# Performance work log

Measured on AMD Instinct MI355X. Metric: run time of the kernel, lower is better.

The kernel has to match this reference:

```python
import jax, jax.numpy as jnp
import numpy as np

M = 65536
INPUT_DIM = 16
OUTPUT_DIM = 64
N = 32          # coordinates transformed by the spline
K = 16          # number of spline bins
MIN_BW = 0.001  # DEFAULT_MIN_BIN_WIDTH
MIN_BH = 0.001  # DEFAULT_MIN_BIN_HEIGHT


def setup_inputs() -> dict:
    key = jax.random.key(0)
    k1, k2, k3, k4 = jax.random.split(key, 4)
    c = jax.random.uniform(k1, (M, INPUT_DIM), jnp.float32)
    z = jax.random.uniform(k2, (M, OUTPUT_DIM), jnp.float32)  # data in [0,1] spline domain
    s_in = OUTPUT_DIM - N + INPUT_DIM  # 48
    s_out = N * (2 * K + 1)            # 1056
    W = jax.random.normal(k3, (s_in, s_out), jnp.float32) * 0.05
    b = jax.random.normal(k4, (s_out,), jnp.float32) * 0.05
    return {"c": c, "z": z, "W": W, "b": b}


def _quadratic_spline(inputs, unnormalized_widths, unnormalized_heights):
    # inputs: [m, n] in [0,1]; unnormalized_widths: [m, n, K]; unnormalized_heights: [m, n, K+1]
    num_bins = unnormalized_widths.shape[-1]

    widths = jax.nn.softmax(unnormalized_widths, axis=-1)
    widths = MIN_BW + (1.0 - MIN_BW * num_bins) * widths

    h = jax.nn.softplus(unnormalized_heights) + 0.001  # [m, n, K+1]
    # (heights have K+1 = num_bins+1 knots, so the 'num_bins-1' padding branch is skipped)
    area = jnp.sum((h[..., :-1] + h[..., 1:]) * 0.5 * widths, axis=-1, keepdims=True)
    heights = h / area
    heights = MIN_BH + (1.0 - MIN_BH) * heights

    cdf = jnp.cumsum((heights[..., :-1] + heights[..., 1:]) * 0.5 * widths, axis=-1)
    cdf = cdf.at[..., -1].set(1.0)
    bin_left_cdf = jnp.pad(cdf, ((0, 0), (0, 0), (1, 0)))  # [m, n, K+1]

    locs = jnp.cumsum(widths, axis=-1).at[..., -1].set(1.0)
    bin_locations = jnp.pad(locs, ((0, 0), (0, 0), (1, 0)))  # [m, n, K+1]

    # nflows torchutils.searchsorted: bump last knot by eps, count knots <= input
    locs_eps = bin_locations.at[..., -1].add(1e-6)
    bin_idx = jnp.sum(inputs[..., None] >= locs_eps, axis=-1) - 1  # [m, n] int

    def gather(arr, idx):
        return jnp.take_along_axis(arr, idx[..., None], axis=-1)[..., 0]

    input_bin_locations = gather(bin_locations, bin_idx)
    input_bin_widths = gather(widths, bin_idx)
    input_left_cdf = gather(bin_left_cdf, bin_idx)
    input_left_heights = gather(heights, bin_idx)
    input_right_heights = gather(heights, bin_idx + 1)

    a = 0.5 * (input_right_heights - input_left_heights) * input_bin_widths
    bq = input_left_heights * input_bin_widths
    cq = input_left_cdf

    alpha = (inputs - input_bin_locations) / input_bin_widths
    outputs = jnp.clip(a * alpha ** 2 + bq * alpha + cq, 0.0, 1.0)
    logabsdet = jnp.log(alpha * (input_right_heights - input_left_heights) + input_left_heights)
    return outputs, logabsdet


def reference(c, z, W, b):
    # forward (reverse=False) branch of QuadraticsSpline.forward
    z1, z2 = z[:, :N], z[:, N:]
    z2c = jnp.concatenate([z2, c], axis=1)
    y = z2c @ W + b                                  # conditioner s (linear)
    sv = y.reshape(y.shape[0], N, 2 * K + 1)
    unnormalized_heights = sv[..., : K + 1]          # first split chunk (size K+1)
    unnormalized_widths = sv[..., K + 1:]            # second chunk (size K)
    x1, log_det = _quadratic_spline(z1, unnormalized_widths, unnormalized_heights)
    x = jnp.concatenate([z2, x1], axis=1)            # note: original concatenates (x2, x1)
    return x, log_det.sum(axis=1)
```

## Files before the change

### kernel.cpp

```cpp
#include <hip/hip_runtime.h>
#include <hip/hip_bf16.h>
#include <math.h>

#define M_ROWS 65536
#define NSPLINE 32
#define BM 64
#define WROWS 16
#define GROUP 4
#define SPB 16
#define NITER (SPB / GROUP)
#define SLOT 40
#define WSLOT (64 * SLOT)
#define WB_ELEMS (32 * 3 * 2 * 64 * 8)

typedef __attribute__((ext_vector_type(8))) _Float16 half8;
typedef __attribute__((ext_vector_type(4))) _Float16 half4;
typedef __attribute__((ext_vector_type(4))) float floatx4;

__device__ __forceinline__ float softplus_fast(float t) {
    float u = t * t;
    float p = fmaf(u, 2.135645e-6f, -2.63517e-5f);
    p = fmaf(u, p, 3.4722222e-4f);
    p = fmaf(u, p, -5.2083333e-3f);
    p = fmaf(u, p, 0.125f);
    p = fmaf(u, p, 0.69314718f);
    return fmaf(t, 0.5f, p);
}

__global__ void pack_W(const float* __restrict__ W, const float* __restrict__ b,
                       _Float16* __restrict__ WH, float* __restrict__ out) {
    int idx = blockIdx.x * 256 + threadIdx.x;
    if (idx < M_ROWS) out[(size_t)M_ROWS * 64 + idx] = 0.0f;
    int j    = idx & 7;
    int lane = (idx >> 3) & 63;
    int half = (idx >> 9) & 1;
    int tmp  = idx >> 10;
    int t    = tmp % 3;
    int sp   = tmp / 3;
    int k  = half * 32 + ((lane >> 4) << 3) + j;
    int cl = t * 16 + (lane & 15);
    float v = 0.0f;
    if (cl < 33 && k <= 48) {
        int col = sp * 33 + cl;
        v = (k < 48) ? W[k * 1056 + col] : b[col];
    }
    WH[idx] = (_Float16)v;
}

__global__ void __launch_bounds__(256) fused_kernel(
    const float* __restrict__ z, const float* __restrict__ c,
    const _Float16* __restrict__ WH, float* __restrict__ out)
{
    __shared__ _Float16 lds[4 * WSLOT];

    const int tid  = threadIdx.x;
    const int w    = tid >> 6;
    const int lane = tid & 63;
    const int q    = lane >> 4;
    const int cc   = lane & 15;
    const int row_base = blockIdx.x * BM + w * WROWS;
    const int sp_base  = blockIdx.y * SPB;
    _Float16* mainA = lds + w * WSLOT;

    if (blockIdx.y == 0) {
        #pragma unroll
        for (int it = 0; it < 2; ++it) {
            int idx = it * 64 + lane;
            int rr  = row_base + (idx >> 3);
            int v4  = idx & 7;
            float4 val = *(const float4*)(z + (size_t)rr * 64 + 32 + v4 * 4);
            *(float4*)(out + (size_t)rr * 64 + v4 * 4) = val;
        }
    }

    half8 a0, a1;
    {
        const float* zr = z + (size_t)(row_base + cc) * 64 + 32;
        float4 v0 = *(const float4*)(zr + q * 8);
        float4 v1 = *(const float4*)(zr + q * 8 + 4);
        a0[0]=(_Float16)v0.x; a0[1]=(_Float16)v0.y;
        a0[2]=(_Float16)v0.z; a0[3]=(_Float16)v0.w;
        a0[4]=(_Float16)v1.x; a0[5]=(_Float16)v1.y;
        a0[6]=(_Float16)v1.z; a0[7]=(_Float16)v1.w;
        if (q < 2) {
            const float* cr = c + (size_t)(row_base + cc) * 16 + q * 8;
            float4 u0 = *(const float4*)cr;
            float4 u1 = *(const float4*)(cr + 4);
            a1[0]=(_Float16)u0.x; a1[1]=(_Float16)u0.y;
            a1[2]=(_Float16)u0.z; a1[3]=(_Float16)u0.w;
            a1[4]=(_Float16)u1.x; a1[5]=(_Float16)u1.y;
            a1[6]=(_Float16)u1.z; a1[7]=(_Float16)u1.w;
        } else {
            #pragma unroll
            for (int j = 0; j < 8; ++j) a1[j] = (_Float16)0.0f;
            if (q == 2) a1[0] = (_Float16)1.0f;
        }
    }

    float zin[NITER];
    {
        const float* zr = z + (size_t)(row_base + cc) * 64 + sp_base + q;
        #pragma unroll
        for (int g = 0; g < NITER; ++g) zin[g] = zr[g * 4];
    }

    float ld_acc = 0.0f;

    #pragma unroll 1
    for (int g = 0; g < NITER; ++g) {
        #pragma unroll
        for (int sp = 0; sp < GROUP; ++sp) {
            const int spg = sp_base + g * GROUP + sp;
            const int task = sp * 16 + cc;
            #pragma unroll
            for (int t = 0; t < 3; ++t) {
                const half8* p = (const half8*)WH + (size_t)(spg * 3 + t) * 128 + lane;
                half8 b0 = p[0];
                half8 b1 = p[64];
                floatx4 acc = {0.f, 0.f, 0.f, 0.f};
                acc = __builtin_amdgcn_mfma_f32_16x16x32_f16(b0, a0, acc, 0, 0, 0);
                acc = __builtin_amdgcn_mfma_f32_16x16x32_f16(b1, a1, acc, 0, 0, 0);
                if (t < 2) {
                    half4 v;
                    v[0] = (_Float16)acc[0]; v[1] = (_Float16)acc[1];
                    v[2] = (_Float16)acc[2]; v[3] = (_Float16)acc[3];
                    *(half4*)(mainA + task * SLOT + t * 16 + q * 4) = v;
                } else if (q == 0) {
                    mainA[task * SLOT + 32] = (_Float16)acc[0];
                }
            }
        }

        const int n = sp_base + g * GROUP + q;
        const _Float16* my = mainA + lane * SLOT;
        const half8* mp = (const half8*)my;
        half8 r0 = mp[0], r1 = mp[1], r2 = mp[2], r3 = mp[3];
        const float p32 = (float)my[32];

        const float in = zin[g];

        float wd[16];
        float sew = 0.f;
        #pragma unroll
        for (int i = 0; i < 7; ++i) {
            float e = __expf((float)r2[1 + i]);
            wd[i] = e; sew += e;
        }
        #pragma unroll
        for (int i = 0; i < 8; ++i) {
            float e = __expf((float)r3[i]);
            wd[7 + i] = e; sew += e;
        }
        {
            float e = __expf(p32);
            wd[15] = e; sew += e;
        }
        const float inv_sew = 0.984f * __builtin_amdgcn_rcpf(sew);
        #pragma unroll
        for (int i = 0; i < 16; ++i) wd[i] = fmaf(wd[i], inv_sew, 0.001f);

        float h[17];
        #pragma unroll
        for (int i = 0; i < 8; ++i) h[i]     = softplus_fast((float)r0[i]) + 0.001f;
        #pragma unroll
        for (int i = 0; i < 8; ++i) h[8 + i] = softplus_fast((float)r1[i]) + 0.001f;
        h[16] = softplus_fast((float)r2[0]) + 0.001f;

        float area2 = 0.f;
        #pragma unroll
        for (int i = 0; i < 16; ++i) area2 = fmaf(h[i] + h[i + 1], wd[i], area2);
        const float inv_area = 1.998f * __builtin_amdgcn_rcpf(area2);
        #pragma unroll
        for (int i = 0; i < 17; ++i) h[i] = fmaf(h[i], inv_area, 0.001f);

        float loc = 0.f, cdfl = 0.f;
        float sel_loc = 0.f, sel_w = wd[0], sel_cdf = 0.f;
        float sel_lh = h[0], sel_rh = h[1];
        #pragma unroll
        for (int bn = 1; bn < 16; ++bn) {
            cdfl = fmaf((h[bn - 1] + h[bn]) * 0.5f, wd[bn - 1], cdfl);
            loc += wd[bn - 1];
            if (in >= loc) {
                sel_loc = loc; sel_w = wd[bn]; sel_cdf = cdfl;
                sel_lh = h[bn]; sel_rh = h[bn + 1];
            }
        }

        const float alpha = (in - sel_loc) / sel_w;
        const float dh    = sel_rh - sel_lh;
        float o = ((0.5f * dh * sel_w) * alpha + sel_lh * sel_w) * alpha + sel_cdf;
        o = fminf(fmaxf(o, 0.0f), 1.0f);
        out[(size_t)(row_base + cc) * 64 + 32 + n] = o;
        ld_acc += __logf(fmaf(alpha, dh, sel_lh));
    }

    ld_acc += __shfl_down(ld_acc, 32, 64);
    ld_acc += __shfl_down(ld_acc, 16, 64);
    if (q == 0)
        atomicAdd(out + (size_t)M_ROWS * 64 + row_base + cc, ld_acc);
}

extern "C" void kernel_launch(void* const* d_in, const int* in_sizes, int n_in,
                              void* d_out, int out_size, void* d_ws, size_t ws_size,
                              hipStream_t stream) {
    const float* c = (const float*)d_in[0];
    const float* z = (const float*)d_in[1];
    const float* W = (const float*)d_in[2];
    const float* b = (const float*)d_in[3];
    float* out = (float*)d_out;
    _Float16* WH = (_Float16*)d_ws;

    pack_W<<<WB_ELEMS / 256, 256, 0, stream>>>(W, b, WH, out);
    fused_kernel<<<dim3(M_ROWS / BM, 2), 256, 0, stream>>>(z, c, WH, out);
}
```

Measured before the change: 120.4 us.

## Process all splines per block and software-pipeline MFMA with spline math

Drops the two-way split of splines across grid.y, so each block handles all 32 spline coordinates. The log-det is now written with a plain store instead of an atomicAdd, which also removes the zeroing pass in pack_W. The GEMM for the next group of splines is computed into registers while the current group's spline math runs, and is stored to LDS afterwards. This hides MFMA and weight-load latency, at the cost of more live registers (12 floatx4 accumulators) and half as many blocks in flight.

```diff
diff --git a/kernel.cpp b/kernel.cpp
--- a/kernel.cpp
+++ b/kernel.cpp
@@ -7,8 +7,7 @@
 #define BM 64
 #define WROWS 16
 #define GROUP 4
-#define SPB 16
-#define NITER (SPB / GROUP)
+#define NITER (NSPLINE / GROUP)
 #define SLOT 40
 #define WSLOT (64 * SLOT)
 #define WB_ELEMS (32 * 3 * 2 * 64 * 8)
@@ -28,9 +27,8 @@
 }
 
 __global__ void pack_W(const float* __restrict__ W, const float* __restrict__ b,
-                       _Float16* __restrict__ WH, float* __restrict__ out) {
+                       _Float16* __restrict__ WH) {
     int idx = blockIdx.x * 256 + threadIdx.x;
-    if (idx < M_ROWS) out[(size_t)M_ROWS * 64 + idx] = 0.0f;
     int j    = idx & 7;
     int lane = (idx >> 3) & 63;
     int half = (idx >> 9) & 1;
@@ -59,18 +57,15 @@
     const int q    = lane >> 4;
     const int cc   = lane & 15;
     const int row_base = blockIdx.x * BM + w * WROWS;
-    const int sp_base  = blockIdx.y * SPB;
     _Float16* mainA = lds + w * WSLOT;
 
-    if (blockIdx.y == 0) {
-        #pragma unroll
-        for (int it = 0; it < 2; ++it) {
-            int idx = it * 64 + lane;
-            int rr  = row_base + (idx >> 3);
-            int v4  = idx & 7;
-            float4 val = *(const float4*)(z + (size_t)rr * 64 + 32 + v4 * 4);
-            *(float4*)(out + (size_t)rr * 64 + v4 * 4) = val;
-        }
+    #pragma unroll
+    for (int it = 0; it < 2; ++it) {
+        int idx = it * 64 + lane;
+        int rr  = row_base + (idx >> 3);
+        int v4  = idx & 7;
+        float4 val = *(const float4*)(z + (size_t)rr * 64 + 32 + v4 * 4);
+        *(float4*)(out + (size_t)rr * 64 + v4 * 4) = val;
     }
 
     half8 a0, a1;
@@ -99,39 +94,55 @@
 
     float zin[NITER];
     {
-        const float* zr = z + (size_t)(row_base + cc) * 64 + sp_base + q;
+        const float* zr = z + (size_t)(row_base + cc) * 64 + q;
         #pragma unroll
         for (int g = 0; g < NITER; ++g) zin[g] = zr[g * 4];
     }
 
-    float ld_acc = 0.0f;
-
-    #pragma unroll 1
-    for (int g = 0; g < NITER; ++g) {
+    floatx4 acc[GROUP][3];
+
+    auto gemm_compute = [&](int g) {
         #pragma unroll
         for (int sp = 0; sp < GROUP; ++sp) {
-            const int spg = sp_base + g * GROUP + sp;
-            const int task = sp * 16 + cc;
+            const int spg = g * GROUP + sp;
             #pragma unroll
             for (int t = 0; t < 3; ++t) {
                 const half8* p = (const half8*)WH + (size_t)(spg * 3 + t) * 128 + lane;
                 half8 b0 = p[0];
                 half8 b1 = p[64];
-                floatx4 acc = {0.f, 0.f, 0.f, 0.f};
-                acc = __builtin_amdgcn_mfma_f32_16x16x32_f16(b0, a0, acc, 0, 0, 0);
-                acc = __builtin_amdgcn_mfma_f32_16x16x32_f16(b1, a1, acc, 0, 0, 0);
-                if (t < 2) {
-                    half4 v;
-                    v[0] = (_Float16)acc[0]; v[1] = (_Float16)acc[1];
-                    v[2] = (_Float16)acc[2]; v[3] = (_Float16)acc[3];
-                    *(half4*)(mainA + task * SLOT + t * 16 + q * 4) = v;
-                } else if (q == 0) {
-                    mainA[task * SLOT + 32] = (_Float16)acc[0];
-                }
+                floatx4 a = {0.f, 0.f, 0.f, 0.f};
+                a = __builtin_amdgcn_mfma_f32_16x16x32_f16(b0, a0, a, 0, 0, 0);
+                a = __builtin_amdgcn_mfma_f32_16x16x32_f16(b1, a1, a, 0, 0, 0);
+                acc[sp][t] = a;
             }
         }
-
-        const int n = sp_base + g * GROUP + q;
+    };
+    auto gemm_store = [&]() {
+        #pragma unroll
+        for (int sp = 0; sp < GROUP; ++sp) {
+            const int task = sp * 16 + cc;
+            #pragma unroll
+            for (int t = 0; t < 2; ++t) {
+                half4 v;
+                v[0] = (_Float16)acc[sp][t][0]; v[1] = (_Float16)acc[sp][t][1];
+                v[2] = (_Float16)acc[sp][t][2]; v[3] = (_Float16)acc[sp][t][3];
+                *(half4*)(mainA + task * SLOT + t * 16 + q * 4) = v;
+            }
+            if (q == 0)
+                mainA[task * SLOT + 32] = (_Float16)acc[sp][2][0];
+        }
+    };
+
+    gemm_compute(0);
+    gemm_store();
+
+    float ld_acc = 0.0f;
+
+    #pragma unroll 1
+    for (int g = 0; g < NITER; ++g) {
+        if (g + 1 < NITER) gemm_compute(g + 1);
+
+        const int n = g * GROUP + q;
         const _Float16* my = mainA + lane * SLOT;
         const half8* mp = (const half8*)my;
         half8 r0 = mp[0], r1 = mp[1], r2 = mp[2], r3 = mp[3];
@@ -192,12 +203,14 @@
         o = fminf(fmaxf(o, 0.0f), 1.0f);
         out[(size_t)(row_base + cc) * 64 + 32 + n] = o;
         ld_acc += __logf(fmaf(alpha, dh, sel_lh));
+
+        if (g + 1 < NITER) gemm_store();
     }
 
     ld_acc += __shfl_down(ld_acc, 32, 64);
     ld_acc += __shfl_down(ld_acc, 16, 64);
     if (q == 0)
-        atomicAdd(out + (size_t)M_ROWS * 64 + row_base + cc, ld_acc);
+        out[(size_t)M_ROWS * 64 + row_base + cc] = ld_acc;
 }
 
 extern "C" void kernel_launch(void* const* d_in, const int* in_sizes, int n_in,
@@ -210,6 +223,6 @@
     float* out = (float*)d_out;
     _Float16* WH = (_Float16*)d_ws;
 
-    pack_W<<<WB_ELEMS / 256, 256, 0, stream>>>(W, b, WH, out);
-    fused_kernel<<<dim3(M_ROWS / BM, 2), 256, 0, stream>>>(z, c, WH, out);
-}
+    pack_W<<<WB_ELEMS / 256, 256, 0, stream>>>(W, b, WH);
+    fused_kernel<<<M_ROWS / BM, 256, 0, stream>>>(z, c, WH, out);
+}
```

Result: slower. 138.9 us (+15.4%).
